# Performance work log

Hardware: AMD Instinct MI355X
Metric: run time of the kernel (lower is better)

## Reference

```python
import jax, jax.numpy as jnp
import numpy as np

N_USERS = 100000
N_ITEMS = 30000
E = 1000000
D = 128
N_LAYERS = 3
W_SELF = 1.0
W_SEEK = 0.5


def _graph_conv(x_src, src, dst, n_src, n_dst, edge_weight=None):
    """DGL GraphConv(weight=False, bias=False, norm='both'):
    out = D_dst^{-1/2} A (D_src^{-1/2} x), edge_weight multiplies messages."""
    ones = jnp.ones(src.shape[0], dtype=x_src.dtype)
    deg_s = jax.ops.segment_sum(ones, src, num_segments=n_src)
    deg_d = jax.ops.segment_sum(ones, dst, num_segments=n_dst)
    norm_s = jnp.where(deg_s > 0, jax.lax.rsqrt(jnp.maximum(deg_s, 1.0)), 0.0)
    norm_d = jnp.where(deg_d > 0, jax.lax.rsqrt(jnp.maximum(deg_d, 1.0)), 0.0)
    m = (x_src * norm_s[:, None])[src]  # [E, D] gather
    if edge_weight is not None:
        m = m * edge_weight[:, None]
    agg = jax.ops.segment_sum(m, dst, num_segments=n_dst)  # [n_dst, D] scatter-add
    return agg * norm_d[:, None]


def setup_inputs() -> dict:
    key = jax.random.key(0)
    ks = jax.random.split(key, 9)
    return {
        'user_emb': jax.random.normal(ks[0], (N_USERS, D), jnp.float32),
        'item_emb': jax.random.normal(ks[1], (N_ITEMS, D), jnp.float32),
        'weight_edge': jax.random.uniform(ks[2], (E,), jnp.float32),
        'ori_u': jax.random.randint(ks[3], (E,), 0, N_USERS, jnp.int32),
        'ori_i': jax.random.randint(ks[4], (E,), 0, N_ITEMS, jnp.int32),
        'seek_u': jax.random.randint(ks[5], (E,), 0, N_USERS, jnp.int32),
        'seek_i': jax.random.randint(ks[6], (E,), 0, N_ITEMS, jnp.int32),
        'dn_u': jax.random.randint(ks[7], (E,), 0, N_USERS, jnp.int32),
        'dn_i': jax.random.randint(ks[8], (E,), 0, N_ITEMS, jnp.int32),
    }


def reference(user_emb, item_emb, weight_edge, ori_u, ori_i, seek_u, seek_i, dn_u, dn_i):
    # ----- first branch: original graph + seek graph fusion -----
    hu, hi = user_emb, item_emb
    for _ in range(N_LAYERS):
        h_user = _graph_conv(hi, ori_i, ori_u, N_ITEMS, N_USERS)
        h_item = _graph_conv(hu, ori_u, ori_i, N_USERS, N_ITEMS)
        h_user_seek = _graph_conv(hi, seek_i, seek_u, N_ITEMS, N_USERS, weight_edge)
        h_item_seek = _graph_conv(hu, seek_u, seek_i, N_USERS, N_ITEMS)
        hu = h_user * W_SELF + h_user_seek * W_SEEK
        hi = h_item * W_SELF + h_item_seek * W_SEEK
    # h_sub1 is an alias of h in the original code (same dict object).
    # ----- second branch: dn graph, seek terms computed from FINAL h (constant per iter) -----
    h_user_seek_f = _graph_conv(hi, seek_i, seek_u, N_ITEMS, N_USERS, weight_edge)
    h_item_seek_f = _graph_conv(hu, seek_u, seek_i, N_USERS, N_ITEMS)
    h1u, h1i = user_emb, item_emb
    for _ in range(N_LAYERS):
        h_user_dn = _graph_conv(h1i, dn_i, dn_u, N_ITEMS, N_USERS)
        h_item_dn = _graph_conv(h1u, dn_u, dn_i, N_USERS, N_ITEMS)
        h1u = h_user_dn * W_SELF + h_user_seek_f * W_SEEK
        h1i = h_item_dn * W_SELF + h_item_seek_f * W_SEEK
    # (h, h_sub1, h1) with h_sub1 == h
    return (hu, hi, hu, hi, h1u, h1i)
```

## Files before the change

### kernel.cpp

```cpp
#include <hip/hip_runtime.h>

#define N_USERS 100000
#define N_ITEMS 30000
#define NE      1000000
#define D       128
#define CHUNK   4096
#define HCHUNK  8192
#define STAGE_B 7424
#define SH_U    9
#define SH_I    7
#define NB_U    ((N_USERS + (1 << SH_U) - 1) >> SH_U)
#define NB_I    ((N_ITEMS + (1 << SH_I) - 1) >> SH_I)

__device__ __forceinline__ unsigned f2bf(float f) {
    unsigned u = __float_as_uint(f);
    return (u + 0x7fffu + ((u >> 16) & 1u)) >> 16;
}
__device__ __forceinline__ float bflo(unsigned v) { return __uint_as_float(v << 16); }
__device__ __forceinline__ float bfhi(unsigned v) { return __uint_as_float(v & 0xffff0000u); }

struct HistArgs { const int* dst[6]; int shift[6]; int* bh; };

__global__ __launch_bounds__(256) void k_bhist(HistArgs a) {
    __shared__ int h[256];
    const int l = blockIdx.y;
    const int* __restrict__ dst = a.dst[l];
    const int sh = a.shift[l];
    const int t = threadIdx.x;
    h[t] = 0;
    __syncthreads();
    const int e0 = blockIdx.x * HCHUNK;
    const int e1 = min(e0 + HCHUNK, NE);
    for (int e = e0 + t; e < e1; e += 256) atomicAdd(&h[dst[e] >> sh], 1);
    __syncthreads();
    if (h[t]) atomicAdd(&a.bh[l * 256 + t], h[t]);
}

__global__ void k_scanB(const int* __restrict__ bh, int* __restrict__ bstart,
                        int* __restrict__ gcur) {
    __shared__ int lds[256];
    const int l = blockIdx.x, t = threadIdx.x;
    const int x = bh[l * 256 + t];
    lds[t] = x;
    __syncthreads();
    for (int o = 1; o < 256; o <<= 1) {
        int add = (t >= o) ? lds[t - o] : 0;
        __syncthreads();
        lds[t] += add;
        __syncthreads();
    }
    const int excl = lds[t] - x;
    bstart[l * 257 + t] = excl;
    gcur[l * 256 + t] = excl;
    if (t == 255) bstart[l * 257 + 256] = lds[t];
}

struct BinList { const int* dst; const int* srcp; const float* w; int shift; int* gcur; int2* tmp; };
struct BinArgs { BinList l[6]; };

__global__ __launch_bounds__(256) void k_binA(BinArgs ba) {
    const BinList L = ba.l[blockIdx.y];
    __shared__ int2 stg[CHUNK];
    __shared__ unsigned char bkt[CHUNK];
    __shared__ int hist[256], sbase[256], scur[256], gbase[256];
    const int t = threadIdx.x;
    const int e0 = blockIdx.x * CHUNK;
    const int ccnt = min(CHUNK, NE - e0);
    hist[t] = 0;
    __syncthreads();
#pragma unroll
    for (int j = 0; j < CHUNK / 256; ++j) {
        const int e = e0 + j * 256 + t;
        if (e < NE) atomicAdd(&hist[L.dst[e] >> L.shift], 1);
    }
    __syncthreads();
    {
        const int x = hist[t];
        sbase[t] = x;
        __syncthreads();
        for (int o = 1; o < 256; o <<= 1) {
            int add = (t >= o) ? sbase[t - o] : 0;
            __syncthreads();
            sbase[t] += add;
            __syncthreads();
        }
        const int excl = sbase[t] - x;
        __syncthreads();
        sbase[t] = excl;
        scur[t] = excl;
        gbase[t] = (x > 0) ? atomicAdd(&L.gcur[t], x) : 0;
    }
    __syncthreads();
#pragma unroll
    for (int j = 0; j < CHUNK / 256; ++j) {
        const int e = e0 + j * 256 + t;
        if (e < NE) {
            const int d = L.dst[e], s = L.srcp[e];
            const int b = d >> L.shift;
            const int p = atomicAdd(&scur[b], 1);
            stg[p] = make_int2(((d & ((1 << L.shift) - 1)) << 17) | s,
                               L.w ? __float_as_int(L.w[e]) : 0);
            bkt[p] = (unsigned char)b;
        }
    }
    __syncthreads();
    for (int i = t; i < ccnt; i += 256) {
        const int b = bkt[i];
        L.tmp[gbase[b] + (i - sbase[b])] = stg[i];
    }
}

struct DegArgs {
    const int2* tmp[6];
    const int* bstart;
    int* rs[6];
    float* rdeg[6];
    int shift[6]; int n[6]; int bofs[7];
};

__global__ __launch_bounds__(256) void k_bdeg(DegArgs a) {
    __shared__ int cnt[512];
    __shared__ int lds[256];
    int l = 0;
    while ((int)blockIdx.x >= a.bofs[l + 1]) ++l;
    const int b = blockIdx.x - a.bofs[l];
    const int sh = a.shift[l], n = a.n[l];
    const int node0 = b << sh;
    const int node1 = min(node0 + (1 << sh), n);
    const int nn = node1 - node0;
    const int bs = a.bstart[l * 257 + b], be = a.bstart[l * 257 + b + 1];
    const int t = threadIdx.x;
    cnt[t] = 0; cnt[t + 256] = 0;
    __syncthreads();
    const int2* __restrict__ tmp = a.tmp[l];
    for (int i = bs + t; i < be; i += 256) atomicAdd(&cnt[((unsigned)tmp[i].x) >> 17], 1);
    __syncthreads();
    const int c0 = cnt[2 * t], c1 = cnt[2 * t + 1];
    lds[t] = c0 + c1;
    __syncthreads();
    for (int o = 1; o < 256; o <<= 1) {
        int add = (t >= o) ? lds[t - o] : 0;
        __syncthreads();
        lds[t] += add;
        __syncthreads();
    }
    const int ep = lds[t] - (c0 + c1);
    int* __restrict__ rs = a.rs[l];
    float* __restrict__ rd = a.rdeg[l];
    if (2 * t < nn) {
        rs[node0 + 2 * t] = bs + ep;
        rd[node0 + 2 * t] = rsqrtf((float)max(c0, 1));
    }
    if (2 * t + 1 < nn) {
        rs[node0 + 2 * t + 1] = bs + ep + c0;
        rd[node0 + 2 * t + 1] = rsqrtf((float)max(c1, 1));
    }
    if (t == 0) rs[node1] = be;
}

struct SortArgs {
    const int2* tmp[6]; int2* outp[6];
    const int* rs[6];
    const float* rdD[6]; const float* rdS[6];
    const int* bstart;
    int shift[6]; int n[6]; int mode[6];
    int bofs[7];
};

__global__ __launch_bounds__(256) void k_binB(SortArgs a) {
    __shared__ int2 stg[STAGE_B];
    __shared__ int lcur[512];
    __shared__ float rdl[512];
    int l = 0;
    while ((int)blockIdx.x >= a.bofs[l + 1]) ++l;
    const int b = blockIdx.x - a.bofs[l];
    const int sh = a.shift[l], n = a.n[l], mode = a.mode[l];
    const int node0 = b << sh;
    const int node1 = min(node0 + (1 << sh), n);
    const int nn = node1 - node0;
    const int bs = a.bstart[l * 257 + b], be = a.bstart[l * 257 + b + 1], cnt = be - bs;
    const int t = threadIdx.x;
    const int* __restrict__ rs = a.rs[l];
    const float* __restrict__ rdD = a.rdD[l];
    for (int k = t; k < nn; k += 256) {
        lcur[k] = rs[node0 + k] - bs;
        rdl[k] = rdD[node0 + k];
    }
    __syncthreads();
    const int2* __restrict__ tmp = a.tmp[l];
    int2* __restrict__ outp = a.outp[l];
    const float* __restrict__ rdS = a.rdS[l];
    if (cnt <= STAGE_B) {
        for (int i = bs + t; i < be; i += 256) {
            const int2 v = tmp[i];
            const int dl = ((unsigned)v.x) >> 17, src = v.x & 0x1FFFF;
            float c = rdl[dl] * rdS[src];
            if (mode == 1) c *= 0.5f * __int_as_float(v.y);
            else if (mode == 2) c *= 0.5f;
            const int slot = atomicAdd(&lcur[dl], 1);
            stg[slot] = make_int2(src << 8, __float_as_int(c));
        }
        __syncthreads();
        for (int i = t; i < cnt; i += 256) outp[bs + i] = stg[i];
    } else {
        for (int i = bs + t; i < be; i += 256) {
            const int2 v = tmp[i];
            const int dl = ((unsigned)v.x) >> 17, src = v.x & 0x1FFFF;
            float c = rdl[dl] * rdS[src];
            if (mode == 1) c *= 0.5f * __int_as_float(v.y);
            else if (mode == 2) c *= 0.5f;
            const int slot = atomicAdd(&lcur[dl], 1);
            outp[bs + slot] = make_int2(src << 8, __float_as_int(c));
        }
    }
}

__global__ void k_tobf16(const float* __restrict__ in, ushort* __restrict__ out, int n4) {
    int i = blockIdx.x * blockDim.x + threadIdx.x;
    if (i >= n4) return;
    float4 v = ((const float4*)in)[i];
    ((uint2*)out)[i] = make_uint2((f2bf(v.y) << 16) | f2bf(v.x),
                                  (f2bf(v.w) << 16) | f2bf(v.z));
}

struct ConvSide {
    const ushort* x;
    const int*  rs1; const int2* p1;
    const int*  rs2; const int2* p2;
    const ushort* base;
    float*  outf; float* outf2;
    ushort* outb;
    int n;
};

__device__ __forceinline__ void accum_list(const char* __restrict__ xb,
                                           const int* __restrict__ rs,
                                           const int2* __restrict__ p,
                                           int row, int laneb,
                                           float& ax, float& ay) {
    const int j0 = rs[row], j1 = rs[row + 1];
    const int lane = laneb >> 2;
    for (int jb = j0; jb < j1; jb += 64) {
        int2 mp = make_int2(0, 0);
        if (jb + lane < j1) mp = p[jb + lane];
        const int cnt = min(64, j1 - jb);
        int t = 0;
        for (; t + 8 <= cnt; t += 8) {
            unsigned v[8]; float c[8];
#pragma unroll
            for (int k = 0; k < 8; ++k) {
                const int so = __builtin_amdgcn_readlane(mp.x, t + k);
                c[k] = __int_as_float(__builtin_amdgcn_readlane(mp.y, t + k));
                v[k] = *(const unsigned*)(xb + so + laneb);
            }
#pragma unroll
            for (int k = 0; k < 8; ++k) {
                ax = fmaf(c[k], bflo(v[k]), ax);
                ay = fmaf(c[k], bfhi(v[k]), ay);
            }
        }
        if (t + 4 <= cnt) {
            unsigned v[4]; float c[4];
#pragma unroll
            for (int k = 0; k < 4; ++k) {
                const int so = __builtin_amdgcn_readlane(mp.x, t + k);
                c[k] = __int_as_float(__builtin_amdgcn_readlane(mp.y, t + k));
                v[k] = *(const unsigned*)(xb + so + laneb);
            }
#pragma unroll
            for (int k = 0; k < 4; ++k) {
                ax = fmaf(c[k], bflo(v[k]), ax);
                ay = fmaf(c[k], bfhi(v[k]), ay);
            }
            t += 4;
        }
        for (; t < cnt; ++t) {
            const int so = __builtin_amdgcn_readlane(mp.x, t);
            const float c = __int_as_float(__builtin_amdgcn_readlane(mp.y, t));
            const unsigned v = *(const unsigned*)(xb + so + laneb);
            ax = fmaf(c, bflo(v), ax);
            ay = fmaf(c, bfhi(v), ay);
        }
    }
}

__global__ void k_conv2(ConvSide A, ConvSide B) {
    int row = (int)((blockIdx.x * blockDim.x + threadIdx.x) >> 6);
    const int lane = threadIdx.x & 63;
    const ConvSide* S = &A;
    if (row >= A.n) {
        row -= A.n;
        if (row >= B.n) return;
        S = &B;
    }
    row = __builtin_amdgcn_readfirstlane(row);
    const int laneb = lane << 2;
    const size_t roff = (size_t)row * D + lane * 2;
    float ax = 0.f, ay = 0.f;
    if (S->base) {
        const unsigned b = *(const unsigned*)(S->base + roff);
        ax = bflo(b); ay = bfhi(b);
    }
    const char* xb = (const char*)S->x;
    accum_list(xb, S->rs1, S->p1, row, laneb, ax, ay);
    if (S->rs2) accum_list(xb, S->rs2, S->p2, row, laneb, ax, ay);
    if (S->outf)  *(float2*)(S->outf  + roff) = make_float2(ax, ay);
    if (S->outf2) *(float2*)(S->outf2 + roff) = make_float2(ax, ay);
    if (S->outb)  *(unsigned*)(S->outb + roff) = (f2bf(ay) << 16) | f2bf(ax);
}

extern "C" void kernel_launch(void* const* d_in, const int* in_sizes, int n_in,
                              void* d_out, int out_size, void* d_ws, size_t ws_size,
                              hipStream_t stream) {
    const float* user_emb = (const float*)d_in[0];
    const float* item_emb = (const float*)d_in[1];
    const float* w_edge   = (const float*)d_in[2];
    const int* ou = (const int*)d_in[3];
    const int* oi = (const int*)d_in[4];
    const int* su = (const int*)d_in[5];
    const int* si = (const int*)d_in[6];
    const int* du = (const int*)d_in[7];
    const int* di = (const int*)d_in[8];
    float* out = (float*)d_out;

    const size_t SZ_U = (size_t)N_USERS * D;
    const size_t SZ_I = (size_t)N_ITEMS * D;

    float* o0 = out;
    float* o1 = o0 + SZ_U;
    float* o2 = o1 + SZ_I;
    float* o3 = o2 + SZ_U;
    float* o4 = o3 + SZ_I;
    float* o5 = o4 + SZ_U;

    ushort* tU0 = (ushort*)o4;  ushort* tU1 = tU0 + SZ_U;
    ushort* tI0 = (ushort*)o5;  ushort* tI1 = tI0 + SZ_I;

    char* ws = (char*)d_ws;
    size_t off = 0;
    auto alloc = [&](size_t bytes) -> void* {
        void* p = ws + off;
        off = (off + bytes + 255) & ~(size_t)255;
        return p;
    };

    int* rOU = (int*)alloc((N_USERS + 1) * 4);
    int* rOI = (int*)alloc((N_ITEMS + 1) * 4);
    int* rSU = (int*)alloc((N_USERS + 1) * 4);
    int* rSI = (int*)alloc((N_ITEMS + 1) * 4);
    int* rDU = (int*)alloc((N_USERS + 1) * 4);
    int* rDI = (int*)alloc((N_ITEMS + 1) * 4);

    float* rdOU = (float*)alloc(N_USERS * 4);
    float* rdOI = (float*)alloc(N_ITEMS * 4);
    float* rdSU = (float*)alloc(N_USERS * 4);
    float* rdSI = (float*)alloc(N_ITEMS * 4);
    float* rdDU = (float*)alloc(N_USERS * 4);
    float* rdDI = (float*)alloc(N_ITEMS * 4);

    size_t bhBegin = off;
    int* bh     = (int*)alloc(6 * 256 * 4);
    size_t bhEnd = off;
    int* bstart = (int*)alloc(6 * 257 * 4);
    int* gcur   = (int*)alloc(6 * 256 * 4);

    int2* pOU = (int2*)alloc((size_t)NE * 8);
    int2* pOI = (int2*)alloc((size_t)NE * 8);
    int2* pSU = (int2*)alloc((size_t)NE * 8);
    int2* pSI = (int2*)alloc((size_t)NE * 8);
    int2* pDU = (int2*)alloc((size_t)NE * 8);
    int2* pDI = (int2*)alloc((size_t)NE * 8);

    int2* qOU = (int2*)alloc((size_t)NE * 8);
    int2* qOI = (int2*)alloc((size_t)NE * 8);
    int2* qSU = (int2*)alloc((size_t)NE * 8);
    int2* qSI = (int2*)alloc((size_t)NE * 8);
    int2* qDU = (int2*)alloc((size_t)NE * 8);
    int2* qDI = (int2*)alloc((size_t)NE * 8);

    ushort* ebU = (ushort*)alloc(SZ_U * 2);
    ushort* ebI = (ushort*)alloc(SZ_I * 2);
    ushort* fUb = (ushort*)alloc(SZ_U * 2);
    ushort* fIb = (ushort*)alloc(SZ_I * 2);

    hipMemsetAsync(ws + bhBegin, 0, bhEnd - bhBegin, stream);
    hipLaunchKernelGGL(k_tobf16, dim3((unsigned)(SZ_U / 4 + 255) / 256), dim3(256), 0, stream,
                       user_emb, ebU, (int)(SZ_U / 4));
    hipLaunchKernelGGL(k_tobf16, dim3((unsigned)(SZ_I / 4 + 255) / 256), dim3(256), 0, stream,
                       item_emb, ebI, (int)(SZ_I / 4));

    HistArgs ha;
    ha.dst[0] = ou; ha.shift[0] = SH_U;
    ha.dst[1] = oi; ha.shift[1] = SH_I;
    ha.dst[2] = su; ha.shift[2] = SH_U;
    ha.dst[3] = si; ha.shift[3] = SH_I;
    ha.dst[4] = du; ha.shift[4] = SH_U;
    ha.dst[5] = di; ha.shift[5] = SH_I;
    ha.bh = bh;
    hipLaunchKernelGGL(k_bhist, dim3((NE + HCHUNK - 1) / HCHUNK, 6), dim3(256), 0, stream, ha);
    hipLaunchKernelGGL(k_scanB, dim3(6), dim3(256), 0, stream, bh, bstart, gcur);

    BinArgs ba;
    ba.l[0] = { ou, oi, nullptr, SH_U, gcur + 0 * 256, qOU };
    ba.l[1] = { oi, ou, nullptr, SH_I, gcur + 1 * 256, qOI };
    ba.l[2] = { su, si, w_edge,  SH_U, gcur + 2 * 256, qSU };
    ba.l[3] = { si, su, nullptr, SH_I, gcur + 3 * 256, qSI };
    ba.l[4] = { du, di, nullptr, SH_U, gcur + 4 * 256, qDU };
    ba.l[5] = { di, du, nullptr, SH_I, gcur + 5 * 256, qDI };
    hipLaunchKernelGGL(k_binA, dim3((NE + CHUNK - 1) / CHUNK, 6), dim3(256), 0, stream, ba);

    int bofs[7];
    {
        int nb[6] = { NB_U, NB_I, NB_U, NB_I, NB_U, NB_I };
        bofs[0] = 0;
        for (int i = 0; i < 6; ++i) bofs[i + 1] = bofs[i] + nb[i];
    }

    DegArgs da;
    da.tmp[0] = qOU; da.rs[0] = rOU; da.rdeg[0] = rdOU; da.shift[0] = SH_U; da.n[0] = N_USERS;
    da.tmp[1] = qOI; da.rs[1] = rOI; da.rdeg[1] = rdOI; da.shift[1] = SH_I; da.n[1] = N_ITEMS;
    da.tmp[2] = qSU; da.rs[2] = rSU; da.rdeg[2] = rdSU; da.shift[2] = SH_U; da.n[2] = N_USERS;
    da.tmp[3] = qSI; da.rs[3] = rSI; da.rdeg[3] = rdSI; da.shift[3] = SH_I; da.n[3] = N_ITEMS;
    da.tmp[4] = qDU; da.rs[4] = rDU; da.rdeg[4] = rdDU; da.shift[4] = SH_U; da.n[4] = N_USERS;
    da.tmp[5] = qDI; da.rs[5] = rDI; da.rdeg[5] = rdDI; da.shift[5] = SH_I; da.n[5] = N_ITEMS;
    da.bstart = bstart;
    for (int i = 0; i < 7; ++i) da.bofs[i] = bofs[i];
    hipLaunchKernelGGL(k_bdeg, dim3(bofs[6]), dim3(256), 0, stream, da);

    SortArgs so;
    so.tmp[0] = qOU; so.outp[0] = pOU; so.rs[0] = rOU; so.rdD[0] = rdOU; so.rdS[0] = rdOI;
    so.shift[0] = SH_U; so.n[0] = N_USERS; so.mode[0] = 0;
    so.tmp[1] = qOI; so.outp[1] = pOI; so.rs[1] = rOI; so.rdD[1] = rdOI; so.rdS[1] = rdOU;
    so.shift[1] = SH_I; so.n[1] = N_ITEMS; so.mode[1] = 0;
    so.tmp[2] = qSU; so.outp[2] = pSU; so.rs[2] = rSU; so.rdD[2] = rdSU; so.rdS[2] = rdSI;
    so.shift[2] = SH_U; so.n[2] = N_USERS; so.mode[2] = 1;
    so.tmp[3] = qSI; so.outp[3] = pSI; so.rs[3] = rSI; so.rdD[3] = rdSI; so.rdS[3] = rdSU;
    so.shift[3] = SH_I; so.n[3] = N_ITEMS; so.mode[3] = 2;
    so.tmp[4] = qDU; so.outp[4] = pDU; so.rs[4] = rDU; so.rdD[4] = rdDU; so.rdS[4] = rdDI;
    so.shift[4] = SH_U; so.n[4] = N_USERS; so.mode[4] = 0;
    so.tmp[5] = qDI; so.outp[5] = pDI; so.rs[5] = rDI; so.rdD[5] = rdDI; so.rdS[5] = rdDU;
    so.shift[5] = SH_I; so.n[5] = N_ITEMS; so.mode[5] = 0;
    so.bstart = bstart;
    for (int i = 0; i < 7; ++i) so.bofs[i] = bofs[i];
    hipLaunchKernelGGL(k_binB, dim3(bofs[6]), dim3(256), 0, stream, so);

    auto mkside = [](const ushort* x, const int* rs1, const int2* p1,
                     const int* rs2, const int2* p2, const ushort* base,
                     float* outf, float* outf2, ushort* outb, int n) {
        ConvSide s; s.x = x; s.rs1 = rs1; s.p1 = p1; s.rs2 = rs2; s.p2 = p2;
        s.base = base; s.outf = outf; s.outf2 = outf2; s.outb = outb; s.n = n;
        return s;
    };
    auto conv2 = [&](const ConvSide& A, const ConvSide& B) {
        const int rows = A.n + B.n;
        dim3 g((unsigned)((rows + 3) / 4)), b(256);
        hipLaunchKernelGGL(k_conv2, g, b, 0, stream, A, B);
    };

    conv2(mkside(ebI, rOU, pOU, rSU, pSU, nullptr, nullptr, nullptr, tU0, N_USERS),
          mkside(ebU, rOI, pOI, rSI, pSI, nullptr, nullptr, nullptr, tI0, N_ITEMS));
    conv2(mkside(tI0, rOU, pOU, rSU, pSU, nullptr, nullptr, nullptr, tU1, N_USERS),
          mkside(tU0, rOI, pOI, rSI, pSI, nullptr, nullptr, nullptr, tI1, N_ITEMS));
    conv2(mkside(tI1, rOU, pOU, rSU, pSU, nullptr, o0, o2, tU0, N_USERS),
          mkside(tU1, rOI, pOI, rSI, pSI, nullptr, o1, o3, tI0, N_ITEMS));

    conv2(mkside(tI0, rSU, pSU, nullptr, nullptr, nullptr, nullptr, nullptr, fUb, N_USERS),
          mkside(tU0, rSI, pSI, nullptr, nullptr, nullptr, nullptr, nullptr, fIb, N_ITEMS));

    conv2(mkside(ebI, rDU, pDU, nullptr, nullptr, fUb, nullptr, nullptr, tU1, N_USERS),
          mkside(ebU, rDI, pDI, nullptr, nullptr, fIb, nullptr, nullptr, tI1, N_ITEMS));
    conv2(mkside(tI1, rDU, pDU, nullptr, nullptr, fUb, nullptr, nullptr, ebU, N_USERS),
          mkside(tU1, rDI, pDI, nullptr, nullptr, fIb, nullptr, nullptr, ebI, N_ITEMS));
    conv2(mkside(ebI, rDU, pDU, nullptr, nullptr, fUb, o4, nullptr, nullptr, N_USERS),
          mkside(ebU, rDI, pDI, nullptr, nullptr, fIb, o5, nullptr, nullptr, N_ITEMS));
}
```

Baseline: 970.8 us.

## Map conv rows to XCDs so each die gathers from one source table

Replaces the linear row-to-workgroup mapping of the conv kernel with an XCD-aware mapping. Blocks are assigned round-robin across the 8 XCDs, so blockIdx&7 picks a die. Four dies handle user rows (gathering item embeddings) and four handle item rows (gathering user embeddings), each die taking a contiguous row chunk. The intent is to keep each die's L2 working set to a single gathered table, improving cache hit rates for the random gathers. The cost is some idle blocks, since the grid is sized by the larger side and item-side blocks exit early, and it relies on the hardware's round-robin block-to-XCD dispatch.

```diff
diff --git a/kernel.cpp b/kernel.cpp
--- a/kernel.cpp
+++ b/kernel.cpp
@@ -284,15 +284,27 @@
     }
 }
 
-__global__ void k_conv2(ConvSide A, ConvSide B) {
-    int row = (int)((blockIdx.x * blockDim.x + threadIdx.x) >> 6);
+#define XU 4
+
+__global__ __launch_bounds__(256) void k_conv2x(ConvSide A, ConvSide B,
+                                                int maxbA, int maxbB) {
+    const int xcd = (int)blockIdx.x & 7;
+    const int idx = (int)blockIdx.x >> 3;
+    const ConvSide* S;
+    int nch, chunk;
+    if (xcd < XU) {
+        if (idx >= maxbA) return;
+        S = &A; nch = XU; chunk = xcd;
+    } else {
+        if (idx >= maxbB) return;
+        S = &B; nch = 8 - XU; chunk = xcd - XU;
+    }
+    const int per = (S->n + nch - 1) / nch;
+    const int r0 = chunk * per;
+    const int r1 = min(r0 + per, S->n);
+    int row = r0 + idx * 4 + (int)(threadIdx.x >> 6);
     const int lane = threadIdx.x & 63;
-    const ConvSide* S = &A;
-    if (row >= A.n) {
-        row -= A.n;
-        if (row >= B.n) return;
-        S = &B;
-    }
+    if (row >= r1) return;
     row = __builtin_amdgcn_readfirstlane(row);
     const int laneb = lane << 2;
     const size_t roff = (size_t)row * D + lane * 2;
@@ -451,26 +463,30 @@
         s.base = base; s.outf = outf; s.outf2 = outf2; s.outb = outb; s.n = n;
         return s;
     };
-    auto conv2 = [&](const ConvSide& A, const ConvSide& B) {
-        const int rows = A.n + B.n;
-        dim3 g((unsigned)((rows + 3) / 4)), b(256);
-        hipLaunchKernelGGL(k_conv2, g, b, 0, stream, A, B);
+    auto conv2x = [&](const ConvSide& A, const ConvSide& B) {
+        const int perA = (A.n + XU - 1) / XU;
+        const int perB = (B.n + (8 - XU) - 1) / (8 - XU);
+        const int maxbA = (perA + 3) / 4;
+        const int maxbB = (perB + 3) / 4;
+        const int nwg = 8 * max(maxbA, maxbB);
+        hipLaunchKernelGGL(k_conv2x, dim3((unsigned)nwg), dim3(256), 0, stream,
+                           A, B, maxbA, maxbB);
     };
 
-    conv2(mkside(ebI, rOU, pOU, rSU, pSU, nullptr, nullptr, nullptr, tU0, N_USERS),
-          mkside(ebU, rOI, pOI, rSI, pSI, nullptr, nullptr, nullptr, tI0, N_ITEMS));
-    conv2(mkside(tI0, rOU, pOU, rSU, pSU, nullptr, nullptr, nullptr, tU1, N_USERS),
-          mkside(tU0, rOI, pOI, rSI, pSI, nullptr, nullptr, nullptr, tI1, N_ITEMS));
-    conv2(mkside(tI1, rOU, pOU, rSU, pSU, nullptr, o0, o2, tU0, N_USERS),
-          mkside(tU1, rOI, pOI, rSI, pSI, nullptr, o1, o3, tI0, N_ITEMS));
-
-    conv2(mkside(tI0, rSU, pSU, nullptr, nullptr, nullptr, nullptr, nullptr, fUb, N_USERS),
-          mkside(tU0, rSI, pSI, nullptr, nullptr, nullptr, nullptr, nullptr, fIb, N_ITEMS));
-
-    conv2(mkside(ebI, rDU, pDU, nullptr, nullptr, fUb, nullptr, nullptr, tU1, N_USERS),
-          mkside(ebU, rDI, pDI, nullptr, nullptr, fIb, nullptr, nullptr, tI1, N_ITEMS));
-    conv2(mkside(tI1, rDU, pDU, nullptr, nullptr, fUb, nullptr, nullptr, ebU, N_USERS),
-          mkside(tU1, rDI, pDI, nullptr, nullptr, fIb, nullptr, nullptr, ebI, N_ITEMS));
-    conv2(mkside(ebI, rDU, pDU, nullptr, nullptr, fUb, o4, nullptr, nullptr, N_USERS),
-          mkside(ebU, rDI, pDI, nullptr, nullptr, fIb, o5, nullptr, nullptr, N_ITEMS));
-}
+    conv2x(mkside(ebI, rOU, pOU, rSU, pSU, nullptr, nullptr, nullptr, tU0, N_USERS),
+           mkside(ebU, rOI, pOI, rSI, pSI, nullptr, nullptr, nullptr, tI0, N_ITEMS));
+    conv2x(mkside(tI0, rOU, pOU, rSU, pSU, nullptr, nullptr, nullptr, tU1, N_USERS),
+           mkside(tU0, rOI, pOI, rSI, pSI, nullptr, nullptr, nullptr, tI1, N_ITEMS));
+    conv2x(mkside(tI1, rOU, pOU, rSU, pSU, nullptr, o0, o2, tU0, N_USERS),
+           mkside(tU1, rOI, pOI, rSI, pSI, nullptr, o1, o3, tI0, N_ITEMS));
+
+    conv2x(mkside(tI0, rSU, pSU, nullptr, nullptr, nullptr, nullptr, nullptr, fUb, N_USERS),
+           mkside(tU0, rSI, pSI, nullptr, nullptr, nullptr, nullptr, nullptr, fIb, N_ITEMS));
+
+    conv2x(mkside(ebI, rDU, pDU, nullptr, nullptr, fUb, nullptr, nullptr, tU1, N_USERS),
+           mkside(ebU, rDI, pDI, nullptr, nullptr, fIb, nullptr, nullptr, tI1, N_ITEMS));
+    conv2x(mkside(tI1, rDU, pDU, nullptr, nullptr, fUb, nullptr, nullptr, ebU, N_USERS),
+           mkside(tU1, rDI, pDI, nullptr, nullptr, fIb, nullptr, nullptr, ebI, N_ITEMS));
+    conv2x(mkside(ebI, rDU, pDU, nullptr, nullptr, fUb, o4, nullptr, nullptr, N_USERS),
+           mkside(ebU, rDI, pDI, nullptr, nullptr, fIb, o5, nullptr, nullptr, N_ITEMS));
+}
```

After: 957.7 us. No clear change (-1.4%).
